# Kernel tuning notes

Measured on AMD Instinct MI355X. Metric: run time of the kernel, lower is better.

## Reference

```python
import jax, jax.numpy as jnp
import numpy as np

N_NODES = 100000
N_EDGES = 3200000


def _gcn_conv(x, src, dst, W, b, n):
    # symmetric GCN normalization with self-loops (PyG GCNConv default)
    deg = jax.ops.segment_sum(jnp.ones_like(dst, dtype=x.dtype), dst, num_segments=n)
    dinv = jnp.where(deg > 0, jax.lax.rsqrt(jnp.maximum(deg, 1e-12)), 0.0)
    norm = dinv[src] * dinv[dst]                       # [E+N]
    h = x @ W                                          # [n, out]
    msg = h[src] * norm[:, None]                       # gather + scale
    out = jax.ops.segment_sum(msg, dst, num_segments=n)  # scatter-add
    return out + b


def setup_inputs() -> dict:
    key = jax.random.key(0)
    k1, k2, k3, k4 = jax.random.split(key, 4)
    feat = jax.random.normal(k1, (N_NODES, 1), dtype=jnp.float32)
    edge_ix = jax.random.randint(k2, (2, N_EDGES), 0, N_NODES, dtype=jnp.int64)
    W1 = jax.random.normal(k3, (1, 32), dtype=jnp.float32) * (1.0 / 1.0)
    b1 = jnp.zeros((32,), dtype=jnp.float32)
    W2 = jax.random.normal(k4, (32, 64), dtype=jnp.float32) * (1.0 / np.sqrt(32.0))
    b2 = jnp.zeros((64,), dtype=jnp.float32)
    return {"feat": feat, "edge_ix": edge_ix, "W1": W1, "b1": b1, "W2": W2, "b2": b2}


def reference(feat, edge_ix, W1, b1, W2, b2):
    n = feat.shape[0]
    # add self loops once; reuse for both layers
    loops = jnp.arange(n, dtype=edge_ix.dtype)
    src = jnp.concatenate([edge_ix[0], loops])
    dst = jnp.concatenate([edge_ix[1], loops])
    x = jax.nn.relu(_gcn_conv(feat, src, dst, W1, b1, n))
    x = jax.nn.relu(_gcn_conv(x, src, dst, W2, b2, n))
    return x
```

## Files before the change

kernel.cpp:

```cpp
#include <hip/hip_runtime.h>


#define TPB 256
#define TPBW 1024
#define NSBMAX 1024
#define SBSZ 256
#define LBITS 8

__global__ void k_detect(const int* __restrict__ e32, int E, int* __restrict__ flag,
                         int* __restrict__ gHist, int NSB) {
    __shared__ int ok;
    if (threadIdx.x == 0) ok = 1;
    __syncthreads();
    for (int i = threadIdx.x; i < NSB; i += TPB) gHist[i] = 0;
    int stride = E / 2048; if (stride < 1) stride = 1;
    bool bad = false;
#pragma unroll
    for (int i = 0; i < 8; ++i) {
        long k = (long)(threadIdx.x * 8 + i) * stride + 1;
        if (k < E && e32[2 * k + 1] != 0) bad = true;
    }
    if (bad) atomicAnd(&ok, 0);
    __syncthreads();
    if (threadIdx.x == 0) *flag = ok;
}

__global__ void k_uv(const float* __restrict__ W1, const float* __restrict__ b1,
                     const float* __restrict__ W2, float* __restrict__ upm,
                     int* __restrict__ bzero) {
    __shared__ float sw[32], sb[32];
    int k = threadIdx.x;
    if (k < 32) { sw[k] = W1[k]; sb[k] = b1[k]; }
    __syncthreads();
    float up = 0.f, um = 0.f;
#pragma unroll
    for (int c = 0; c < 32; ++c) {
        float w = sw[c];
        float w2 = W2[c * 64 + k];
        up = fmaf(fmaxf(w, 0.f), w2, up);
        um = fmaf(fmaxf(-w, 0.f), w2, um);
    }
    upm[k] = up;
    upm[64 + k] = um;
    if (k == 0) {
        int z = 1;
        for (int c = 0; c < 32; ++c) if (sb[c] != 0.f) z = 0;
        *bzero = z;
    }
}

__global__ void k_hist(const int* __restrict__ e32, const int* __restrict__ flag,
                       int E, int NSB, int* __restrict__ gHist) {
    __shared__ int sh[NSBMAX];
    for (int i = threadIdx.x; i < NSB; i += TPBW) sh[i] = 0;
    __syncthreads();
    int f = *flag;
    long stride = (long)gridDim.x * TPBW;
    for (long e = (long)blockIdx.x * TPBW + threadIdx.x; e < E; e += stride) {
        int d = e32[((long)E + e) << f];
        atomicAdd(&sh[d >> LBITS], 1);
    }
    __syncthreads();
    for (int i = threadIdx.x; i < NSB; i += TPBW)
        if (sh[i]) atomicAdd(&gHist[i], sh[i]);
}

__global__ void k_scan(const int* __restrict__ gHist, int NSB, int E,
                       int* __restrict__ base, int* __restrict__ cursor) {
    __shared__ int s[TPB];
    int K = (NSB + TPB - 1) / TPB;
    int t = threadIdx.x;
    int i0 = t * K;
    int tot = 0;
    for (int k = 0; k < K; ++k) { int i = i0 + k; if (i < NSB) tot += gHist[i]; }
    s[t] = tot;
    __syncthreads();
    for (int off = 1; off < TPB; off <<= 1) {
        int v = s[t];
        int u = (t >= off) ? s[t - off] : 0;
        __syncthreads();
        s[t] = v + u;
        __syncthreads();
    }
    int run = s[t] - tot;
    for (int k = 0; k < K; ++k) {
        int i = i0 + k;
        if (i < NSB) { int h = gHist[i]; base[i] = run; cursor[i] = run; run += h; }
    }
    if (t == 0) base[NSB] = E;
}

__global__ void k_part(const int* __restrict__ e32, const int* __restrict__ flag,
                       int E, int NSB, int* __restrict__ cursor,
                       unsigned int* __restrict__ P, int chunk) {
    __shared__ int sh[NSBMAX];
    int c0 = blockIdx.x * chunk;
    int c1 = c0 + chunk; if (c1 > E) c1 = E;
    for (int i = threadIdx.x; i < NSB; i += TPBW) sh[i] = 0;
    __syncthreads();
    int f = *flag;
    for (int e = c0 + threadIdx.x; e < c1; e += TPBW) {
        int d = e32[((long)E + e) << f];
        atomicAdd(&sh[d >> LBITS], 1);
    }
    __syncthreads();
    for (int i = threadIdx.x; i < NSB; i += TPBW) {
        int c = sh[i];
        sh[i] = c ? atomicAdd(&cursor[i], c) : 0;
    }
    __syncthreads();
    int sshift = 32 - LBITS;
    for (int e = c0 + threadIdx.x; e < c1; e += TPBW) {
        long ee = (long)e << f;
        int s = e32[ee];
        int d = e32[(((long)E) << f) + ee];
        int b = d >> LBITS;
        int pos = atomicAdd(&sh[b], 1);
        P[pos] = (unsigned)s | ((unsigned)(d & (SBSZ - 1)) << sshift);
    }
}

__global__ void k_deg(const unsigned int* __restrict__ P, const int* __restrict__ base,
                      int n, const float* __restrict__ feat,
                      float* __restrict__ dinv, float* __restrict__ g) {
    __shared__ int cnt[SBSZ];
    int b = blockIdx.x, t = threadIdx.x;
    if (t < SBSZ) cnt[t] = 0;
    __syncthreads();
    int p0 = base[b], p1 = base[b + 1];
    int sshift = 32 - LBITS;
    for (int p = p0 + t; p < p1; p += TPBW)
        atomicAdd(&cnt[P[p] >> sshift], 1);
    __syncthreads();
    int v = (b << LBITS) + t;
    if (t < SBSZ && v < n) {
        float di = rsqrtf((float)(cnt[t] + 1));
        dinv[v] = di;
        g[v] = di * feat[v];
    }
}

__global__ void k_aggA(const unsigned int* __restrict__ P, const int* __restrict__ base,
                       int n, const float* __restrict__ g,
                       const float* __restrict__ dinv, const int* __restrict__ bzero,
                       float2* __restrict__ q2, float2* __restrict__ pd,
                       float* __restrict__ Yagg) {
    __shared__ float A[SBSZ];
    int b = blockIdx.x, t = threadIdx.x;
    int v = (b << LBITS) + t;
    if (t < SBSZ) A[t] = (v < n) ? g[v] : 0.f;
    __syncthreads();
    int p0 = base[b], p1 = base[b + 1];
    int sshift = 32 - LBITS;
    unsigned smask = (1u << sshift) - 1;
    for (int p = p0 + t; p < p1; p += TPBW) {
        unsigned e = P[p];
        atomicAdd(&A[e >> sshift], g[e & smask]);
    }
    __syncthreads();
    if (t < SBSZ && v < n) {
        float di = dinv[v];
        float px = di * A[t];
        q2[v] = make_float2(di * fmaxf(px, 0.f), di * fmaxf(-px, 0.f));
        if (!*bzero) {
            pd[v] = make_float2(px, di);
            float4* Y = (float4*)(Yagg + (size_t)v * 32);
#pragma unroll
            for (int i = 0; i < 8; ++i) Y[i] = make_float4(0.f, 0.f, 0.f, 0.f);
        }
    }
}

__global__ void k_aggT(const unsigned int* __restrict__ P, const int* __restrict__ base,
                       int n, const float2* __restrict__ q2,
                       const float* __restrict__ dinv, const float* __restrict__ upm,
                       const float* __restrict__ b2, const int* __restrict__ bzero,
                       float* __restrict__ out) {
    if (!*bzero) return;
    __shared__ float Sp[SBSZ], Sm[SBSZ], Sd[SBSZ];
    __shared__ float su[192];
    int b = blockIdx.x, t = threadIdx.x;
    int v0 = b << LBITS;
    int v = v0 + t;
    if (t < SBSZ) {
        if (v < n) { float2 q = q2[v]; Sp[t] = q.x; Sm[t] = q.y; Sd[t] = dinv[v]; }
        else       { Sp[t] = 0.f; Sm[t] = 0.f; Sd[t] = 0.f; }
    }
    if (t < 192) su[t] = (t < 128) ? upm[t] : b2[t - 128];
    __syncthreads();
    int p0 = base[b], p1 = base[b + 1];
    int sshift = 32 - LBITS;
    unsigned smask = (1u << sshift) - 1;
    for (int p = p0 + t; p < p1; p += TPBW) {
        unsigned e = P[p];
        float2 q = q2[e & smask];
        int l = e >> sshift;
        atomicAdd(&Sp[l], q.x);
        atomicAdd(&Sm[l], q.y);
    }
    __syncthreads();
    int nv = n - v0; if (nv > SBSZ) nv = SBSZ; if (nv < 0) nv = 0;
    for (int o = t; o < nv * 64; o += TPBW) {
        int vl = o >> 6, k = o & 63;
        float r = fmaf(Sd[vl], fmaf(Sp[vl], su[k], Sm[vl] * su[64 + k]), su[128 + k]);
        out[(size_t)(v0 + vl) * 64 + k] = fmaxf(r, 0.f);
    }
}

__global__ void k_aggY(const int* __restrict__ e32, const int* __restrict__ flag,
                       int E, const int* __restrict__ bzero,
                       const float2* __restrict__ pd,
                       const float* __restrict__ W1, const float* __restrict__ b1,
                       float* __restrict__ Yagg) {
    if (*bzero) return;
    __shared__ float sw[32], sb[32];
    if (threadIdx.x < 32) { sw[threadIdx.x] = W1[threadIdx.x]; sb[threadIdx.x] = b1[threadIdx.x]; }
    __syncthreads();
    int sh = *flag;
    long stride = (long)gridDim.x * TPB;
    for (long e = (long)blockIdx.x * TPB + threadIdx.x; e < E; e += stride) {
        int s = e32[e << sh];
        int d = e32[((long)E + e) << sh];
        float2 p = pd[s];
#pragma unroll
        for (int c = 0; c < 32; ++c) {
            float y = p.y * fmaxf(fmaf(sw[c], p.x, sb[c] * p.y), 0.f);
            atomicAdd(&Yagg[(size_t)d * 32 + c], y);
        }
    }
}

__global__ void k_final_gen(const float2* __restrict__ pd, const float* __restrict__ Yagg,
                            const float* __restrict__ W1, const float* __restrict__ b1,
                            const float* __restrict__ W2, const float* __restrict__ b2,
                            const int* __restrict__ bzero, int n, float* __restrict__ out) {
    if (*bzero) return;
    __shared__ float sW[32 * 64];
    __shared__ float sb2[64];
    __shared__ float sagg[8][33];
    int t = threadIdx.x;
    for (int i = t; i < 32 * 64; i += TPB) sW[i] = W2[i];
    if (t < 64) sb2[t] = b2[t];
    int vl = t >> 5, c = t & 31;
    int nblk = (n + 7) / 8;
    for (int blk = blockIdx.x; blk < nblk; blk += gridDim.x) {
        int v = blk * 8 + vl;
        float a = 0.f;
        if (v < n) {
            float2 p = pd[v];
            float dv = p.y;
            float yv = fmaxf(fmaf(W1[c], p.x, b1[c] * p.y), 0.f);
            a = dv * (dv * yv + Yagg[(size_t)v * 32 + c]);
        }
        __syncthreads();
        sagg[vl][c] = a;
        __syncthreads();
        if (v < n) {
            float o0 = sb2[c], o1 = sb2[c + 32];
#pragma unroll
            for (int j = 0; j < 32; ++j) {
                float x = sagg[vl][j];
                o0 += x * sW[j * 64 + c];
                o1 += x * sW[j * 64 + 32 + c];
            }
            out[(size_t)v * 64 + c]      = fmaxf(o0, 0.f);
            out[(size_t)v * 64 + 32 + c] = fmaxf(o1, 0.f);
        }
    }
}

static inline size_t align256(size_t x) { return (x + 255) & ~(size_t)255; }

extern "C" void kernel_launch(void* const* d_in, const int* in_sizes, int n_in,
                              void* d_out, int out_size, void* d_ws, size_t ws_size,
                              hipStream_t stream) {
    const float* feat = (const float*)d_in[0];
    const int*   e32  = (const int*)d_in[1];
    const float* W1   = (const float*)d_in[2];
    const float* b1   = (const float*)d_in[3];
    const float* W2   = (const float*)d_in[4];
    const float* b2   = (const float*)d_in[5];
    float* out = (float*)d_out;

    int n = in_sizes[0];
    int E = in_sizes[1] / 2;

    int NSB = (n + SBSZ - 1) >> LBITS;

    char* w = (char*)d_ws;
    size_t off = 0;
    auto alloc = [&](size_t bytes) -> char* { char* p = w + off; off = align256(off + bytes); return p; };
    unsigned int* P = (unsigned int*)alloc((size_t)E * 4);
    int*    gHist = (int*)alloc((size_t)NSB * 4);
    int*    base  = (int*)alloc((size_t)(NSB + 1) * 4);
    int*    cursor= (int*)alloc((size_t)NSB * 4);
    float*  dinv  = (float*)alloc((size_t)n * 4);
    float*  g     = (float*)alloc((size_t)n * 4);
    float2* q2    = (float2*)alloc((size_t)n * 8);
    float2* pd    = (float2*)alloc((size_t)n * 8);
    float*  upm   = (float*)alloc(128 * 4);
    int*    flag  = (int*)alloc(4);
    int*    bzero = (int*)alloc(4);
    float*  Yagg  = (float*)alloc((size_t)n * 32 * 4);

    int chunk = (E + 255) / 256;
    int gC = (E + chunk - 1) / chunk;

    hipLaunchKernelGGL(k_detect,    dim3(1),    dim3(TPB),  0, stream, e32, E, flag, gHist, NSB);
    hipLaunchKernelGGL(k_uv,        dim3(1),    dim3(64),   0, stream, W1, b1, W2, upm, bzero);
    hipLaunchKernelGGL(k_hist,      dim3(128),  dim3(TPBW), 0, stream, e32, flag, E, NSB, gHist);
    hipLaunchKernelGGL(k_scan,      dim3(1),    dim3(TPB),  0, stream, gHist, NSB, E, base, cursor);
    hipLaunchKernelGGL(k_part,      dim3(gC),   dim3(TPBW), 0, stream, e32, flag, E, NSB, cursor, P, chunk);
    hipLaunchKernelGGL(k_deg,       dim3(NSB),  dim3(TPBW), 0, stream, P, base, n, feat, dinv, g);
    hipLaunchKernelGGL(k_aggA,      dim3(NSB),  dim3(TPBW), 0, stream, P, base, n, g, dinv, bzero, q2, pd, Yagg);
    hipLaunchKernelGGL(k_aggT,      dim3(NSB),  dim3(TPBW), 0, stream, P, base, n, q2, dinv, upm, b2, bzero, out);
    hipLaunchKernelGGL(k_aggY,      dim3(512),  dim3(TPB),  0, stream, e32, flag, E, bzero, pd, W1, b1, Yagg);
    hipLaunchKernelGGL(k_final_gen, dim3(1024), dim3(TPB),  0, stream, pd, Yagg, W1, b1, W2, b2, bzero, n, out);
}
```

Before: 133.4 us.

## Split per-superbucket aggregation across multiple blocks with partial-sum reduction kernels

Each destination superbucket's edge range is now split across SPLIT=4 smaller 256-thread blocks. Each block writes per-node partial counts or sums to global buffers, and new elementwise kernels (prep1, prep2, out) reduce those partials. This raises parallelism beyond the ~391 superbucket blocks and makes the output write fully coalesced. Layer-2 aggregation now scatters one signed value into positive or negative accumulators instead of gathering a float2, and the histogram grid is doubled. The cost is extra launches and global traffic for the partial buffers.

```diff
diff --git a/kernel.cpp b/kernel.cpp
--- a/kernel.cpp
+++ b/kernel.cpp
@@ -6,6 +6,7 @@
 #define NSBMAX 1024
 #define SBSZ 256
 #define LBITS 8
+#define SPLIT 4
 
 __global__ void k_detect(const int* __restrict__ e32, int E, int* __restrict__ flag,
                          int* __restrict__ gHist, int NSB) {
@@ -120,91 +121,118 @@
     }
 }
 
-__global__ void k_deg(const unsigned int* __restrict__ P, const int* __restrict__ base,
-                      int n, const float* __restrict__ feat,
-                      float* __restrict__ dinv, float* __restrict__ g) {
+__global__ void k_degS(const unsigned int* __restrict__ P, const int* __restrict__ base,
+                       int n, int* __restrict__ cntP) {
     __shared__ int cnt[SBSZ];
-    int b = blockIdx.x, t = threadIdx.x;
-    if (t < SBSZ) cnt[t] = 0;
-    __syncthreads();
-    int p0 = base[b], p1 = base[b + 1];
+    int bb = blockIdx.x / SPLIT, pp = blockIdx.x % SPLIT;
+    int t = threadIdx.x;
+    cnt[t] = 0;
+    __syncthreads();
+    int p0 = base[bb], len = base[bb + 1] - p0;
+    int s0 = p0 + (int)((long)len * pp / SPLIT);
+    int s1 = p0 + (int)((long)len * (pp + 1) / SPLIT);
     int sshift = 32 - LBITS;
-    for (int p = p0 + t; p < p1; p += TPBW)
+    for (int p = s0 + t; p < s1; p += TPB)
         atomicAdd(&cnt[P[p] >> sshift], 1);
     __syncthreads();
-    int v = (b << LBITS) + t;
-    if (t < SBSZ && v < n) {
-        float di = rsqrtf((float)(cnt[t] + 1));
-        dinv[v] = di;
-        g[v] = di * feat[v];
-    }
-}
-
-__global__ void k_aggA(const unsigned int* __restrict__ P, const int* __restrict__ base,
-                       int n, const float* __restrict__ g,
-                       const float* __restrict__ dinv, const int* __restrict__ bzero,
-                       float2* __restrict__ q2, float2* __restrict__ pd,
-                       float* __restrict__ Yagg) {
+    int v = (bb << LBITS) + t;
+    if (v < n) cntP[pp * n + v] = cnt[t];
+}
+
+__global__ void k_prep1(const int* __restrict__ cntP, const float* __restrict__ feat,
+                        int n, float* __restrict__ dinv, float* __restrict__ g) {
+    int v = blockIdx.x * TPB + threadIdx.x;
+    if (v >= n) return;
+    int c = 0;
+#pragma unroll
+    for (int pp = 0; pp < SPLIT; ++pp) c += cntP[pp * n + v];
+    float di = rsqrtf((float)(c + 1));
+    dinv[v] = di;
+    g[v] = di * feat[v];
+}
+
+__global__ void k_aggAS(const unsigned int* __restrict__ P, const int* __restrict__ base,
+                        int n, const float* __restrict__ g, float* __restrict__ AP) {
     __shared__ float A[SBSZ];
-    int b = blockIdx.x, t = threadIdx.x;
-    int v = (b << LBITS) + t;
-    if (t < SBSZ) A[t] = (v < n) ? g[v] : 0.f;
-    __syncthreads();
-    int p0 = base[b], p1 = base[b + 1];
+    int bb = blockIdx.x / SPLIT, pp = blockIdx.x % SPLIT;
+    int t = threadIdx.x;
+    A[t] = 0.f;
+    __syncthreads();
+    int p0 = base[bb], len = base[bb + 1] - p0;
+    int s0 = p0 + (int)((long)len * pp / SPLIT);
+    int s1 = p0 + (int)((long)len * (pp + 1) / SPLIT);
     int sshift = 32 - LBITS;
     unsigned smask = (1u << sshift) - 1;
-    for (int p = p0 + t; p < p1; p += TPBW) {
+    for (int p = s0 + t; p < s1; p += TPB) {
         unsigned e = P[p];
         atomicAdd(&A[e >> sshift], g[e & smask]);
     }
     __syncthreads();
-    if (t < SBSZ && v < n) {
-        float di = dinv[v];
-        float px = di * A[t];
-        q2[v] = make_float2(di * fmaxf(px, 0.f), di * fmaxf(-px, 0.f));
-        if (!*bzero) {
-            pd[v] = make_float2(px, di);
-            float4* Y = (float4*)(Yagg + (size_t)v * 32);
-#pragma unroll
-            for (int i = 0; i < 8; ++i) Y[i] = make_float4(0.f, 0.f, 0.f, 0.f);
-        }
-    }
-}
-
-__global__ void k_aggT(const unsigned int* __restrict__ P, const int* __restrict__ base,
-                       int n, const float2* __restrict__ q2,
-                       const float* __restrict__ dinv, const float* __restrict__ upm,
-                       const float* __restrict__ b2, const int* __restrict__ bzero,
-                       float* __restrict__ out) {
-    if (!*bzero) return;
-    __shared__ float Sp[SBSZ], Sm[SBSZ], Sd[SBSZ];
-    __shared__ float su[192];
-    int b = blockIdx.x, t = threadIdx.x;
-    int v0 = b << LBITS;
-    int v = v0 + t;
-    if (t < SBSZ) {
-        if (v < n) { float2 q = q2[v]; Sp[t] = q.x; Sm[t] = q.y; Sd[t] = dinv[v]; }
-        else       { Sp[t] = 0.f; Sm[t] = 0.f; Sd[t] = 0.f; }
-    }
-    if (t < 192) su[t] = (t < 128) ? upm[t] : b2[t - 128];
-    __syncthreads();
-    int p0 = base[b], p1 = base[b + 1];
+    int v = (bb << LBITS) + t;
+    if (v < n) AP[pp * n + v] = A[t];
+}
+
+__global__ void k_prep2(const float* __restrict__ AP, const float* __restrict__ g,
+                        const float* __restrict__ dinv, int n, const int* __restrict__ bzero,
+                        float* __restrict__ qs, float2* __restrict__ pd,
+                        float* __restrict__ Yagg) {
+    int v = blockIdx.x * TPB + threadIdx.x;
+    if (v >= n) return;
+    float A = g[v];
+#pragma unroll
+    for (int pp = 0; pp < SPLIT; ++pp) A += AP[pp * n + v];
+    float di = dinv[v];
+    float px = di * A;
+    qs[v] = di * px;
+    if (!*bzero) {
+        pd[v] = make_float2(px, di);
+        float4* Y = (float4*)(Yagg + (size_t)v * 32);
+#pragma unroll
+        for (int i = 0; i < 8; ++i) Y[i] = make_float4(0.f, 0.f, 0.f, 0.f);
+    }
+}
+
+__global__ void k_aggTS(const unsigned int* __restrict__ P, const int* __restrict__ base,
+                        int n, const float* __restrict__ qs, float2* __restrict__ SP2) {
+    __shared__ float Sp[SBSZ], Sm[SBSZ];
+    int bb = blockIdx.x / SPLIT, pp = blockIdx.x % SPLIT;
+    int t = threadIdx.x;
+    Sp[t] = 0.f; Sm[t] = 0.f;
+    __syncthreads();
+    int p0 = base[bb], len = base[bb + 1] - p0;
+    int s0 = p0 + (int)((long)len * pp / SPLIT);
+    int s1 = p0 + (int)((long)len * (pp + 1) / SPLIT);
     int sshift = 32 - LBITS;
     unsigned smask = (1u << sshift) - 1;
-    for (int p = p0 + t; p < p1; p += TPBW) {
+    for (int p = s0 + t; p < s1; p += TPB) {
         unsigned e = P[p];
-        float2 q = q2[e & smask];
+        float q = qs[e & smask];
         int l = e >> sshift;
-        atomicAdd(&Sp[l], q.x);
-        atomicAdd(&Sm[l], q.y);
-    }
-    __syncthreads();
-    int nv = n - v0; if (nv > SBSZ) nv = SBSZ; if (nv < 0) nv = 0;
-    for (int o = t; o < nv * 64; o += TPBW) {
-        int vl = o >> 6, k = o & 63;
-        float r = fmaf(Sd[vl], fmaf(Sp[vl], su[k], Sm[vl] * su[64 + k]), su[128 + k]);
-        out[(size_t)(v0 + vl) * 64 + k] = fmaxf(r, 0.f);
-    }
+        float* addr = (q >= 0.f) ? &Sp[l] : &Sm[l];
+        atomicAdd(addr, fabsf(q));
+    }
+    __syncthreads();
+    int v = (bb << LBITS) + t;
+    if (v < n) SP2[pp * n + v] = make_float2(Sp[t], Sm[t]);
+}
+
+__global__ void k_out(const float* __restrict__ qs, const float* __restrict__ dinv,
+                      const float2* __restrict__ SP2, const float* __restrict__ upm,
+                      const float* __restrict__ b2, const int* __restrict__ bzero,
+                      int n, float* __restrict__ out) {
+    if (!*bzero) return;
+    __shared__ float su[192];
+    if (threadIdx.x < 192) su[threadIdx.x] = (threadIdx.x < 128) ? upm[threadIdx.x] : b2[threadIdx.x - 128];
+    __syncthreads();
+    int o = blockIdx.x * TPB + threadIdx.x;
+    if (o >= n * 64) return;
+    int v = o >> 6, k = o & 63;
+    float qv = qs[v];
+    float Sp = fmaxf(qv, 0.f), Sm = fmaxf(-qv, 0.f);
+#pragma unroll
+    for (int pp = 0; pp < SPLIT; ++pp) { float2 s = SP2[pp * n + v]; Sp += s.x; Sm += s.y; }
+    float r = fmaf(dinv[v], fmaf(Sp, su[k], Sm * su[64 + k]), su[128 + k]);
+    out[o] = fmaxf(r, 0.f);
 }
 
 __global__ void k_aggY(const int* __restrict__ e32, const int* __restrict__ flag,
@@ -294,9 +322,12 @@
     int*    gHist = (int*)alloc((size_t)NSB * 4);
     int*    base  = (int*)alloc((size_t)(NSB + 1) * 4);
     int*    cursor= (int*)alloc((size_t)NSB * 4);
+    int*    cntP  = (int*)alloc((size_t)SPLIT * n * 4);
+    float*  AP    = (float*)alloc((size_t)SPLIT * n * 4);
+    float2* SP2   = (float2*)alloc((size_t)SPLIT * n * 8);
     float*  dinv  = (float*)alloc((size_t)n * 4);
     float*  g     = (float*)alloc((size_t)n * 4);
-    float2* q2    = (float2*)alloc((size_t)n * 8);
+    float*  qs    = (float*)alloc((size_t)n * 4);
     float2* pd    = (float2*)alloc((size_t)n * 8);
     float*  upm   = (float*)alloc(128 * 4);
     int*    flag  = (int*)alloc(4);
@@ -305,15 +336,21 @@
 
     int chunk = (E + 255) / 256;
     int gC = (E + chunk - 1) / chunk;
+    int gN = (n + TPB - 1) / TPB;
+    int gS = NSB * SPLIT;
+    int gO = (n * 64 + TPB - 1) / TPB;
 
     hipLaunchKernelGGL(k_detect,    dim3(1),    dim3(TPB),  0, stream, e32, E, flag, gHist, NSB);
     hipLaunchKernelGGL(k_uv,        dim3(1),    dim3(64),   0, stream, W1, b1, W2, upm, bzero);
-    hipLaunchKernelGGL(k_hist,      dim3(128),  dim3(TPBW), 0, stream, e32, flag, E, NSB, gHist);
+    hipLaunchKernelGGL(k_hist,      dim3(256),  dim3(TPBW), 0, stream, e32, flag, E, NSB, gHist);
     hipLaunchKernelGGL(k_scan,      dim3(1),    dim3(TPB),  0, stream, gHist, NSB, E, base, cursor);
     hipLaunchKernelGGL(k_part,      dim3(gC),   dim3(TPBW), 0, stream, e32, flag, E, NSB, cursor, P, chunk);
-    hipLaunchKernelGGL(k_deg,       dim3(NSB),  dim3(TPBW), 0, stream, P, base, n, feat, dinv, g);
-    hipLaunchKernelGGL(k_aggA,      dim3(NSB),  dim3(TPBW), 0, stream, P, base, n, g, dinv, bzero, q2, pd, Yagg);
-    hipLaunchKernelGGL(k_aggT,      dim3(NSB),  dim3(TPBW), 0, stream, P, base, n, q2, dinv, upm, b2, bzero, out);
+    hipLaunchKernelGGL(k_degS,      dim3(gS),   dim3(TPB),  0, stream, P, base, n, cntP);
+    hipLaunchKernelGGL(k_prep1,     dim3(gN),   dim3(TPB),  0, stream, cntP, feat, n, dinv, g);
+    hipLaunchKernelGGL(k_aggAS,     dim3(gS),   dim3(TPB),  0, stream, P, base, n, g, AP);
+    hipLaunchKernelGGL(k_prep2,     dim3(gN),   dim3(TPB),  0, stream, AP, g, dinv, n, bzero, qs, pd, Yagg);
+    hipLaunchKernelGGL(k_aggTS,     dim3(gS),   dim3(TPB),  0, stream, P, base, n, qs, SP2);
+    hipLaunchKernelGGL(k_out,       dim3(gO),   dim3(TPB),  0, stream, qs, dinv, SP2, upm, b2, bzero, n, out);
     hipLaunchKernelGGL(k_aggY,      dim3(512),  dim3(TPB),  0, stream, e32, flag, E, bzero, pd, W1, b1, Yagg);
     hipLaunchKernelGGL(k_final_gen, dim3(1024), dim3(TPB),  0, stream, pd, Yagg, W1, b1, W2, b2, bzero, n, out);
 }
```

Measured after the change: 130.7 us. -2.0%, faster.
